# Optimization experiments

Measured on AMD Instinct MI355X. Metric: run time of the kernel, lower is better.

Reference implementation:

```python
import jax, jax.numpy as jnp
import numpy as np

C = 256
H = 4
D = C // H
SCALE = D ** -0.5
EPS = 1e-5


def _lin(x, W, b):
    # torch nn.Linear: y = x @ W.T + b, W: [out, in]
    return x @ W.T + b


def _heads(x):
    B, N, _ = x.shape
    return x.reshape(B, N, H, D).transpose(0, 2, 1, 3)  # [B,H,N,D]


def _merge(x):
    B, h, N, d = x.shape
    return x.transpose(0, 2, 1, 3).reshape(B, N, h * d)


def _attn(q, k, v):
    # q,k,v: [B,H,N,D]; materializes [B,H,N,N] scores like the original
    scores = jnp.einsum('bhnd,bhmd->bhnm', q, k) * SCALE
    p = jax.nn.softmax(scores, axis=-1)
    return jnp.einsum('bhnm,bhmd->bhnd', p, v)


def setup_inputs() -> dict:
    key = jax.random.key(0)
    ks = jax.random.split(key, 20)
    B, N = 4, 4096
    s = 0.02
    inp = {
        'f_freq': jax.random.normal(ks[0], (B, N, C), jnp.float32),
        'f_spat': jax.random.normal(ks[1], (B, N, C), jnp.float32),
        'Wqf': jax.random.normal(ks[2], (C, C), jnp.float32) * s,
        'bqf': jnp.zeros((C,), jnp.float32),
        'Wks': jax.random.normal(ks[3], (C, C), jnp.float32) * s,
        'bks': jnp.zeros((C,), jnp.float32),
        'Wvs': jax.random.normal(ks[4], (C, C), jnp.float32) * s,
        'bvs': jnp.zeros((C,), jnp.float32),
        'Wqs': jax.random.normal(ks[5], (C, C), jnp.float32) * s,
        'bqs': jnp.zeros((C,), jnp.float32),
        'Wkf': jax.random.normal(ks[6], (C, C), jnp.float32) * s,
        'bkf': jnp.zeros((C,), jnp.float32),
        'Wvf': jax.random.normal(ks[7], (C, C), jnp.float32) * s,
        'bvf': jnp.zeros((C,), jnp.float32),
        'Wp': jax.random.normal(ks[8], (C, 2 * C), jnp.float32) * s,
        'bp': jnp.zeros((C,), jnp.float32),
        'gamma': jnp.ones((C,), jnp.float32),
        'beta': jnp.zeros((C,), jnp.float32),
    }
    return inp


def reference(f_freq, f_spat, Wqf, bqf, Wks, bks, Wvs, bvs, Wqs, bqs,
              Wkf, bkf, Wvf, bvf, Wp, bp, gamma, beta):
    # direction 1: freq queries attend to spatial keys/values
    q_f = _heads(_lin(f_freq, Wqf, bqf))
    k_s = _heads(_lin(f_spat, Wks, bks))
    v_s = _heads(_lin(f_spat, Wvs, bvs))
    out_f2s = _merge(_attn(q_f, k_s, v_s))
    # direction 2: spatial queries attend to freq keys/values
    q_s = _heads(_lin(f_spat, Wqs, bqs))
    k_f = _heads(_lin(f_freq, Wkf, bkf))
    v_f = _heads(_lin(f_freq, Wvf, bvf))
    out_s2f = _merge(_attn(q_s, k_f, v_f))
    fused = _lin(jnp.concatenate([out_f2s, out_s2f], axis=-1), Wp, bp)
    # LayerNorm over last dim
    mu = jnp.mean(fused, axis=-1, keepdims=True)
    var = jnp.var(fused, axis=-1, keepdims=True)
    fused = (fused - mu) * jax.lax.rsqrt(var + EPS) * gamma + beta
    return fused
```

## Files before the change

kernel.cpp:

```cpp
#include <hip/hip_runtime.h>
#include <hip/hip_bf16.h>

typedef __attribute__((ext_vector_type(4))) float floatx4;
typedef __attribute__((ext_vector_type(8))) short shortx8;

#define MFMA(a, b, c) __builtin_amdgcn_mfma_f32_16x16x32_bf16(a, b, c, 0, 0, 0)

static constexpr int MTOT = 16384;
static constexpr int NSEQ = 4096;
static constexpr int CD = 256;
static constexpr float SEXP = 0.18033688011112042f;

__device__ __forceinline__ unsigned short f2bf(float f) {
  unsigned int u = __float_as_uint(f);
  u += 0x7fffu + ((u >> 16) & 1u);
  return (unsigned short)(u >> 16);
}

__device__ __forceinline__ shortx8 ld8(const unsigned short* p) {
  return *reinterpret_cast<const shortx8*>(p);
}

__device__ __forceinline__ void gl_lds16(const unsigned short* g, unsigned short* l) {
  __builtin_amdgcn_global_load_lds(
      (const __attribute__((address_space(1))) unsigned int*)g,
      (__attribute__((address_space(3))) unsigned int*)l, 16, 0, 0);
}

__global__ __launch_bounds__(256) void cast_x(const float* __restrict__ s0,
                                              const float* __restrict__ s1,
                                              unsigned short* __restrict__ d0,
                                              unsigned short* __restrict__ d1) {
  const float* src = blockIdx.y ? s1 : s0;
  unsigned short* dst = blockIdx.y ? d1 : d0;
  int i = (blockIdx.x * 256 + threadIdx.x) * 4;
  float4 v = *reinterpret_cast<const float4*>(src + i);
  ushort4 o;
  o.x = f2bf(v.x); o.y = f2bf(v.y); o.z = f2bf(v.z); o.w = f2bf(v.w);
  *reinterpret_cast<ushort4*>(dst + i) = o;
}

struct WSrc { const float* p[8]; };
__global__ __launch_bounds__(256) void cast_w(WSrc srcs, unsigned short* __restrict__ dst) {
  const int j = blockIdx.y;
  const float* src = srcs.p[j];
  int i = (blockIdx.x * 256 + threadIdx.x) * 4;
  float4 v = *reinterpret_cast<const float4*>(src + i);
  ushort4 o;
  o.x = f2bf(v.x); o.y = f2bf(v.y); o.z = f2bf(v.z); o.w = f2bf(v.w);
  *reinterpret_cast<ushort4*>(dst + j * 65536 + i) = o;
}

struct BiasPtrs { const float* p[6]; };

__global__ __launch_bounds__(256) void qkv_gemm(const unsigned short* __restrict__ Xf,
                                                const unsigned short* __restrict__ Xs,
                                                const unsigned short* __restrict__ W6,
                                                BiasPtrs bias6,
                                                unsigned short* __restrict__ Yout) {
  const int j = blockIdx.y;
  const unsigned short* X = ((14 >> j) & 1) ? Xs : Xf;
  const unsigned short* W = W6 + j * 65536;
  const float* bias = bias6.p[j];
  const float sc = (j == 0 || j == 3) ? SEXP : 1.0f;
  unsigned short* Y = Yout + (size_t)j * MTOT * CD;

  const int wave = threadIdx.x >> 6, lane = threadIdx.x & 63;
  const int col = lane & 15, quad = lane >> 4;
  const int m0 = blockIdx.x * 32;
  const int o0 = wave * 64;

  floatx4 acc[2][4];
  for (int mt = 0; mt < 2; ++mt)
    for (int f = 0; f < 4; ++f) acc[mt][f] = floatx4{0.f, 0.f, 0.f, 0.f};

  for (int k0 = 0; k0 < CD; k0 += 32) {
    shortx8 a[2], bb[4];
    for (int mt = 0; mt < 2; ++mt)
      a[mt] = ld8(X + (size_t)(m0 + mt * 16 + col) * CD + k0 + quad * 8);
    for (int f = 0; f < 4; ++f)
      bb[f] = ld8(W + (size_t)(o0 + f * 16 + col) * CD + k0 + quad * 8);
    for (int mt = 0; mt < 2; ++mt)
      for (int f = 0; f < 4; ++f)
        acc[mt][f] = MFMA(a[mt], bb[f], acc[mt][f]);
  }
  for (int mt = 0; mt < 2; ++mt)
    for (int f = 0; f < 4; ++f) {
      const int oc = o0 + f * 16 + col;
      const float bv = bias[oc];
      for (int r = 0; r < 4; ++r)
        Y[(size_t)(m0 + mt * 16 + quad * 4 + r) * CD + oc] = f2bf((acc[mt][f][r] + bv) * sc);
    }
}

__global__ __launch_bounds__(256) void vtrans(const unsigned short* __restrict__ qkv,
                                              unsigned short* __restrict__ Vt) {
  __shared__ unsigned short tile[64][65];
  const int pb = blockIdx.y;
  const int dir = pb >> 4, b = (pb >> 2) & 3, h = pb & 3;
  const size_t SZ = (size_t)MTOT * CD;
  const unsigned short* V = qkv + (size_t)dir * 3 * SZ + 2 * SZ;
  const int n0 = blockIdx.x * 64;
  const int t = threadIdx.x;
  const int dcol = t & 63, nrow = t >> 6;
  for (int nn = 0; nn < 64; nn += 4)
    tile[nn + nrow][dcol] = V[(size_t)(b * NSEQ + n0 + nn + nrow) * CD + h * 64 + dcol];
  __syncthreads();
  const int ncol = t & 63, drow = t >> 6;
  unsigned short* dst = Vt + (size_t)pb * 64 * NSEQ;
  for (int dd = 0; dd < 64; dd += 4)
    dst[(size_t)(dd + drow) * NSEQ + n0 + ncol] = tile[ncol][dd + drow];
}

__global__ __launch_bounds__(256, 2) void attn_kernel(const unsigned short* __restrict__ qkv,
                                                      const unsigned short* __restrict__ Vt,
                                                      unsigned short* __restrict__ Oout) {
  __shared__ unsigned short smem[16384];
  const size_t SZ = (size_t)MTOT * CD;
  const int pb = blockIdx.y;
  const int dir = pb >> 4, b = (pb >> 2) & 3, h4 = pb & 3;
  const unsigned short* Q = qkv + (size_t)dir * 3 * SZ;
  const unsigned short* K = Q + SZ;
  const unsigned short* VT = Vt + (size_t)pb * 64 * NSEQ;
  unsigned short* O = Oout + (size_t)dir * SZ;

  const int wave = threadIdx.x >> 6, lane = threadIdx.x & 63;
  const int col = lane & 15, quad = lane >> 4;
  const int rowbase = b * NSEQ;
  const int cb = h4 * 64;
  const int q0 = blockIdx.x * 256 + wave * 64;

  shortx8 qf[4][2];
  for (int mt = 0; mt < 4; ++mt)
    for (int c = 0; c < 2; ++c)
      qf[mt][c] = ld8(Q + (size_t)(rowbase + q0 + mt * 16 + col) * CD + cb + c * 32 + quad * 8);

  floatx4 oacc[4][4];
  floatx4 lacc[4];
  for (int mt = 0; mt < 4; ++mt) {
    for (int d = 0; d < 4; ++d) oacc[mt][d] = floatx4{0.f, 0.f, 0.f, 0.f};
    lacc[mt] = floatx4{0.f, 0.f, 0.f, 0.f};
  }
  shortx8 ones;
  for (int i = 0; i < 8; ++i) ones[i] = (short)0x3F80;

  const int gp = 8 * (col >> 2) + (col & 3);
  const int swb = 2 * (col & 3);

  int kbase[2][2], vbase[2][4];
  for (int t = 0; t < 2; ++t)
    for (int c = 0; c < 2; ++c)
      kbase[t][c] = (gp + 4 * t) * 64 + ((c * 4 + quad + swb) & 7) * 8;
  for (int h = 0; h < 2; ++h)
    for (int db = 0; db < 4; ++db)
      vbase[h][db] = (db * 16 + col) * 64 + ((h * 4 + quad + swb) & 7) * 8;

  const int r8 = lane >> 3;
  const int cg = (lane - 2 * r8) & 7;

  const unsigned short* pk = K + (size_t)(rowbase + wave * 16 + r8) * CD + cb + cg * 8;
  const unsigned short* pv = VT + (size_t)(wave * 16 + r8) * NSEQ + cg * 8;
  unsigned short* lk = &smem[wave * 1024];
  unsigned short* lv = &smem[8192 + wave * 1024];

#define STAGE(BUF)                                  \
  do {                                              \
    gl_lds16(pk, lk + (BUF) * 4096);                \
    gl_lds16(pk + 8 * CD, lk + (BUF) * 4096 + 512); \
    gl_lds16(pv, lv + (BUF) * 4096);                \
    gl_lds16(pv + 8 * NSEQ, lv + (BUF) * 4096 + 512);\
    pk += 64 * CD;                                  \
    pv += 64;                                       \
  } while (0)

  STAGE(0);
  __syncthreads();

  int buf = 0;
  for (int kt = 0; kt < NSEQ; kt += 64, buf ^= 1) {
    if (kt + 64 < NSEQ) STAGE(buf ^ 1);

    for (int h = 0; h < 2; ++h) {
      shortx8 kf[2][2], vf[4];
      const int kb = buf * 4096 + h * 2048;
      for (int t = 0; t < 2; ++t)
        for (int c = 0; c < 2; ++c) kf[t][c] = ld8(&smem[kb + kbase[t][c]]);
      const int vb = 8192 + buf * 4096;
      for (int db = 0; db < 4; ++db) vf[db] = ld8(&smem[vb + vbase[h][db]]);

      for (int mt = 0; mt < 4; ++mt) {
        floatx4 z = floatx4{0.f, 0.f, 0.f, 0.f};
        floatx4 st0 = MFMA(kf[0][0], qf[mt][0], z);
        st0 = MFMA(kf[0][1], qf[mt][1], st0);
        floatx4 st1 = MFMA(kf[1][0], qf[mt][0], z);
        st1 = MFMA(kf[1][1], qf[mt][1], st1);
        float p[8];
        for (int r = 0; r < 4; ++r) {
          p[r]     = __builtin_amdgcn_exp2f(st0[r]);
          p[4 + r] = __builtin_amdgcn_exp2f(st1[r]);
        }
        union { shortx8 s8; unsigned int u[4]; } pu;
        for (int w = 0; w < 4; ++w)
          pu.u[w] = __builtin_amdgcn_perm(__float_as_uint(p[2 * w + 1]),
                                          __float_as_uint(p[2 * w]), 0x07060302u);
        lacc[mt] = MFMA(ones, pu.s8, lacc[mt]);
        for (int db = 0; db < 4; ++db)
          oacc[mt][db] = MFMA(vf[db], pu.s8, oacc[mt][db]);
      }
    }
    __syncthreads();
  }
#undef STAGE

  for (int mt = 0; mt < 4; ++mt) {
    const float inv = 1.0f / lacc[mt][0];
    for (int db = 0; db < 4; ++db) {
      ushort4 o4;
      o4.x = f2bf(oacc[mt][db][0] * inv);
      o4.y = f2bf(oacc[mt][db][1] * inv);
      o4.z = f2bf(oacc[mt][db][2] * inv);
      o4.w = f2bf(oacc[mt][db][3] * inv);
      *reinterpret_cast<ushort4*>(
          O + (size_t)(rowbase + q0 + mt * 16 + col) * CD + cb + db * 16 + quad * 4) = o4;
    }
  }
}

__global__ __launch_bounds__(256) void final_ln(const unsigned short* __restrict__ O1,
                                                const unsigned short* __restrict__ O2,
                                                const unsigned short* __restrict__ Wp,
                                                const float* __restrict__ bp,
                                                const float* __restrict__ gamma,
                                                const float* __restrict__ beta,
                                                float* __restrict__ out) {
  __shared__ float ssum[4][32], ssq[4][32];
  const int wave = threadIdx.x >> 6, lane = threadIdx.x & 63;
  const int col = lane & 15, quad = lane >> 4;
  const int m0 = blockIdx.x * 32;
  const int o0 = wave * 64;

  floatx4 acc[2][4];
  for (int mt = 0; mt < 2; ++mt)
    for (int f = 0; f < 4; ++f) acc[mt][f] = floatx4{0.f, 0.f, 0.f, 0.f};

  for (int kk = 0; kk < 16; ++kk) {
    const unsigned short* src = (kk < 8) ? O1 : O2;
    const int k0 = (kk & 7) * 32;
    shortx8 a[2], bb[4];
    for (int mt = 0; mt < 2; ++mt)
      a[mt] = ld8(src + (size_t)(m0 + mt * 16 + col) * CD + k0 + quad * 8);
    for (int f = 0; f < 4; ++f)
      bb[f] = ld8(Wp + (size_t)(o0 + f * 16 + col) * 512 + kk * 32 + quad * 8);
    for (int mt = 0; mt < 2; ++mt)
      for (int f = 0; f < 4; ++f)
        acc[mt][f] = MFMA(a[mt], bb[f], acc[mt][f]);
  }

  float vals[2][4][4];
  for (int mt = 0; mt < 2; ++mt)
    for (int f = 0; f < 4; ++f) {
      const float bv = bp[o0 + f * 16 + col];
      for (int r = 0; r < 4; ++r) vals[mt][f][r] = acc[mt][f][r] + bv;
    }

  for (int mt = 0; mt < 2; ++mt)
    for (int r = 0; r < 4; ++r) {
      float s = 0.f, q = 0.f;
      for (int f = 0; f < 4; ++f) { float v = vals[mt][f][r]; s += v; q += v * v; }
      for (int d = 1; d < 16; d <<= 1) { s += __shfl_xor(s, d); q += __shfl_xor(q, d); }
      if (col == 0) {
        ssum[wave][mt * 16 + quad * 4 + r] = s;
        ssq[wave][mt * 16 + quad * 4 + r] = q;
      }
    }
  __syncthreads();
  for (int mt = 0; mt < 2; ++mt)
    for (int r = 0; r < 4; ++r) {
      const int rl = mt * 16 + quad * 4 + r;
      const float S = ssum[0][rl] + ssum[1][rl] + ssum[2][rl] + ssum[3][rl];
      const float Qs = ssq[0][rl] + ssq[1][rl] + ssq[2][rl] + ssq[3][rl];
      const float mean = S * (1.0f / 256.0f);
      const float var = Qs * (1.0f / 256.0f) - mean * mean;
      const float rs = rsqrtf(var + 1e-5f);
      for (int f = 0; f < 4; ++f) {
        const int oc = o0 + f * 16 + col;
        out[(size_t)(m0 + rl) * CD + oc] = (vals[mt][f][r] - mean) * rs * gamma[oc] + beta[oc];
      }
    }
}

extern "C" void kernel_launch(void* const* d_in, const int* in_sizes, int n_in,
                              void* d_out, int out_size, void* d_ws, size_t ws_size,
                              hipStream_t stream) {
  const float* f_freq = (const float*)d_in[0];
  const float* f_spat = (const float*)d_in[1];
  const float* Wqf = (const float*)d_in[2];  const float* bqf = (const float*)d_in[3];
  const float* Wks = (const float*)d_in[4];  const float* bks = (const float*)d_in[5];
  const float* Wvs = (const float*)d_in[6];  const float* bvs = (const float*)d_in[7];
  const float* Wqs = (const float*)d_in[8];  const float* bqs = (const float*)d_in[9];
  const float* Wkf = (const float*)d_in[10]; const float* bkf = (const float*)d_in[11];
  const float* Wvf = (const float*)d_in[12]; const float* bvf = (const float*)d_in[13];
  const float* Wp  = (const float*)d_in[14]; const float* bp  = (const float*)d_in[15];
  const float* gamma = (const float*)d_in[16];
  const float* beta  = (const float*)d_in[17];
  float* out = (float*)d_out;

  const size_t SZ = (size_t)MTOT * CD;
  unsigned short* Xf  = (unsigned short*)d_ws;
  unsigned short* Xs  = Xf + SZ;
  unsigned short* W6  = Xs + SZ;
  unsigned short* WpB = W6 + 6 * 65536;
  unsigned short* QKV = WpB + 131072;
  unsigned short* O1  = QKV + 6 * SZ;
  unsigned short* O2  = O1 + SZ;
  unsigned short* Vt  = Xf;

  cast_x<<<dim3(4096, 2), 256, 0, stream>>>(f_freq, f_spat, Xf, Xs);
  WSrc ws8 = {{Wqf, Wks, Wvs, Wqs, Wkf, Wvf, Wp, Wp + 65536}};
  cast_w<<<dim3(64, 8), 256, 0, stream>>>(ws8, W6);

  BiasPtrs bias6 = {{bqf, bks, bvs, bqs, bkf, bvf}};
  qkv_gemm<<<dim3(512, 6), 256, 0, stream>>>(Xf, Xs, W6, bias6, QKV);

  vtrans<<<dim3(64, 32), 256, 0, stream>>>(QKV, Vt);

  attn_kernel<<<dim3(16, 32), 256, 0, stream>>>(QKV, Vt, O1);

  final_ln<<<512, 256, 0, stream>>>(O1, O2, WpB, bp, gamma, beta, out);
}
```

Measured before the change: 339.0 us.

## Tile QKV GEMM through LDS double buffer and halve attention query tile

The QKV projection GEMM now stages 128x32 tiles of X and W into LDS with async global-to-LDS loads and a double buffer. Each block computes a 128x128 output with 2x2 waves, replacing the old per-wave direct global loads that reloaded W for every 32-row block. The attention kernel drops from 64 to 32 query rows per wave and launches twice as many blocks, with launch bounds raised to 4 blocks per CU for more parallelism and occupancy. The trade-off is that each K/V tile staged in LDS is reused by fewer queries, so attention does more K/V staging traffic overall.

```diff
diff --git a/kernel.cpp b/kernel.cpp
--- a/kernel.cpp
+++ b/kernel.cpp
@@ -53,12 +53,14 @@
 
 struct BiasPtrs { const float* p[6]; };
 
-__global__ __launch_bounds__(256) void qkv_gemm(const unsigned short* __restrict__ Xf,
-                                                const unsigned short* __restrict__ Xs,
-                                                const unsigned short* __restrict__ W6,
-                                                BiasPtrs bias6,
-                                                unsigned short* __restrict__ Yout) {
-  const int j = blockIdx.y;
+__global__ __launch_bounds__(256, 4) void qkv_gemm(const unsigned short* __restrict__ Xf,
+                                                   const unsigned short* __restrict__ Xs,
+                                                   const unsigned short* __restrict__ W6,
+                                                   BiasPtrs bias6,
+                                                   unsigned short* __restrict__ Yout) {
+  __shared__ unsigned short smem[16384];
+  const int j = blockIdx.y >> 1;
+  const int o128 = (blockIdx.y & 1) * 128;
   const unsigned short* X = ((14 >> j) & 1) ? Xs : Xf;
   const unsigned short* W = W6 + j * 65536;
   const float* bias = bias6.p[j];
@@ -67,29 +69,54 @@
 
   const int wave = threadIdx.x >> 6, lane = threadIdx.x & 63;
   const int col = lane & 15, quad = lane >> 4;
-  const int m0 = blockIdx.x * 32;
-  const int o0 = wave * 64;
-
-  floatx4 acc[2][4];
-  for (int mt = 0; mt < 2; ++mt)
+  const int m0 = blockIdx.x * 128;
+  const int mq = (wave & 1) * 64, oq = (wave >> 1) * 64;
+
+  const int rA = lane >> 2, cA = lane & 3;
+  const unsigned short* pA = X + (size_t)(m0 + wave * 32 + rA) * CD + cA * 8;
+  const unsigned short* pB = W + (size_t)(o128 + wave * 32 + rA) * CD + cA * 8;
+  unsigned short* lA = &smem[wave * 1024];
+  unsigned short* lB = &smem[8192 + wave * 1024];
+
+#define QSTAGE(BUF)                                   \
+  do {                                                \
+    gl_lds16(pA, lA + (BUF) * 4096);                  \
+    gl_lds16(pA + 16 * CD, lA + (BUF) * 4096 + 512);  \
+    gl_lds16(pB, lB + (BUF) * 4096);                  \
+    gl_lds16(pB + 16 * CD, lB + (BUF) * 4096 + 512);  \
+    pA += 32;                                         \
+    pB += 32;                                         \
+  } while (0)
+
+  floatx4 acc[4][4];
+  for (int mt = 0; mt < 4; ++mt)
     for (int f = 0; f < 4; ++f) acc[mt][f] = floatx4{0.f, 0.f, 0.f, 0.f};
 
-  for (int k0 = 0; k0 < CD; k0 += 32) {
-    shortx8 a[2], bb[4];
-    for (int mt = 0; mt < 2; ++mt)
-      a[mt] = ld8(X + (size_t)(m0 + mt * 16 + col) * CD + k0 + quad * 8);
+  QSTAGE(0);
+  __syncthreads();
+
+  int buf = 0;
+  for (int ks = 0; ks < 8; ++ks, buf ^= 1) {
+    if (ks + 1 < 8) QSTAGE(buf ^ 1);
+    shortx8 a[4], b[4];
+    for (int mt = 0; mt < 4; ++mt)
+      a[mt] = ld8(&smem[buf * 4096 + (mq + mt * 16 + col) * 32 + quad * 8]);
     for (int f = 0; f < 4; ++f)
-      bb[f] = ld8(W + (size_t)(o0 + f * 16 + col) * CD + k0 + quad * 8);
-    for (int mt = 0; mt < 2; ++mt)
+      b[f] = ld8(&smem[8192 + buf * 4096 + (oq + f * 16 + col) * 32 + quad * 8]);
+    for (int mt = 0; mt < 4; ++mt)
       for (int f = 0; f < 4; ++f)
-        acc[mt][f] = MFMA(a[mt], bb[f], acc[mt][f]);
-  }
-  for (int mt = 0; mt < 2; ++mt)
+        acc[mt][f] = MFMA(a[mt], b[f], acc[mt][f]);
+    __syncthreads();
+  }
+#undef QSTAGE
+
+  for (int mt = 0; mt < 4; ++mt)
     for (int f = 0; f < 4; ++f) {
-      const int oc = o0 + f * 16 + col;
+      const int oc = o128 + oq + f * 16 + col;
       const float bv = bias[oc];
       for (int r = 0; r < 4; ++r)
-        Y[(size_t)(m0 + mt * 16 + quad * 4 + r) * CD + oc] = f2bf((acc[mt][f][r] + bv) * sc);
+        Y[(size_t)(m0 + mq + mt * 16 + quad * 4 + r) * CD + oc] =
+            f2bf((acc[mt][f][r] + bv) * sc);
     }
 }
 
@@ -112,7 +139,7 @@
     dst[(size_t)(dd + drow) * NSEQ + n0 + ncol] = tile[ncol][dd + drow];
 }
 
-__global__ __launch_bounds__(256, 2) void attn_kernel(const unsigned short* __restrict__ qkv,
+__global__ __launch_bounds__(256, 4) void attn_kernel(const unsigned short* __restrict__ qkv,
                                                       const unsigned short* __restrict__ Vt,
                                                       unsigned short* __restrict__ Oout) {
   __shared__ unsigned short smem[16384];
@@ -128,16 +155,16 @@
   const int col = lane & 15, quad = lane >> 4;
   const int rowbase = b * NSEQ;
   const int cb = h4 * 64;
-  const int q0 = blockIdx.x * 256 + wave * 64;
-
-  shortx8 qf[4][2];
-  for (int mt = 0; mt < 4; ++mt)
+  const int q0 = blockIdx.x * 128 + wave * 32;
+
+  shortx8 qf[2][2];
+  for (int mt = 0; mt < 2; ++mt)
     for (int c = 0; c < 2; ++c)
       qf[mt][c] = ld8(Q + (size_t)(rowbase + q0 + mt * 16 + col) * CD + cb + c * 32 + quad * 8);
 
-  floatx4 oacc[4][4];
-  floatx4 lacc[4];
-  for (int mt = 0; mt < 4; ++mt) {
+  floatx4 oacc[2][4];
+  floatx4 lacc[2];
+  for (int mt = 0; mt < 2; ++mt) {
     for (int d = 0; d < 4; ++d) oacc[mt][d] = floatx4{0.f, 0.f, 0.f, 0.f};
     lacc[mt] = floatx4{0.f, 0.f, 0.f, 0.f};
   }
@@ -188,7 +215,7 @@
       const int vb = 8192 + buf * 4096;
       for (int db = 0; db < 4; ++db) vf[db] = ld8(&smem[vb + vbase[h][db]]);
 
-      for (int mt = 0; mt < 4; ++mt) {
+      for (int mt = 0; mt < 2; ++mt) {
         floatx4 z = floatx4{0.f, 0.f, 0.f, 0.f};
         floatx4 st0 = MFMA(kf[0][0], qf[mt][0], z);
         st0 = MFMA(kf[0][1], qf[mt][1], st0);
@@ -212,7 +239,7 @@
   }
 #undef STAGE
 
-  for (int mt = 0; mt < 4; ++mt) {
+  for (int mt = 0; mt < 2; ++mt) {
     const float inv = 1.0f / lacc[mt][0];
     for (int db = 0; db < 4; ++db) {
       ushort4 o4;
@@ -320,11 +347,11 @@
   cast_w<<<dim3(64, 8), 256, 0, stream>>>(ws8, W6);
 
   BiasPtrs bias6 = {{bqf, bks, bvs, bqs, bkf, bvf}};
-  qkv_gemm<<<dim3(512, 6), 256, 0, stream>>>(Xf, Xs, W6, bias6, QKV);
+  qkv_gemm<<<dim3(128, 12), 256, 0, stream>>>(Xf, Xs, W6, bias6, QKV);
 
   vtrans<<<dim3(64, 32), 256, 0, stream>>>(QKV, Vt);
 
-  attn_kernel<<<dim3(16, 32), 256, 0, stream>>>(QKV, Vt, O1);
+  attn_kernel<<<dim3(32, 32), 256, 0, stream>>>(QKV, Vt, O1);
 
   final_ln<<<512, 256, 0, stream>>>(O1, O2, WpB, bp, gamma, beta, out);
 }
```

Measured after the change: 308.3 us. 9.1% less time.
